# Performance work log

Hardware: AMD Instinct MI355X
Metric: run time of the kernel (lower is better)

Reference implementation:

```python
import jax, jax.numpy as jnp
import numpy as np

IN_DIM = 256
OUT_DIM = 256
B, N, E = 8, 1024, 262144
K_RATIO = 0.5
BN_EPS = 1e-5


def _xavier(key, shape):
    fan_in, fan_out = shape[1], shape[0]
    lim = float(np.sqrt(6.0 / (fan_in + fan_out)))
    return jax.random.uniform(key, shape, jnp.float32, -lim, lim)


def setup_inputs() -> dict:
    key = jax.random.key(0)
    ks = jax.random.split(key, 10)
    x = jax.random.normal(ks[0], (B, N, IN_DIM), jnp.float32)
    edges = jax.random.randint(ks[1], (2, E), 0, B * N, jnp.int64 if jax.config.jax_enable_x64 else jnp.int32)
    return {
        "x": x,
        "edges": edges,
        "att_proj_w": _xavier(ks[2], (OUT_DIM, IN_DIM)),
        "att_proj_b": jnp.zeros((OUT_DIM,), jnp.float32),
        "att_map_w": _xavier(ks[3], (1, OUT_DIM)).reshape(OUT_DIM),
        "pwa_w": _xavier(ks[4], (OUT_DIM, IN_DIM)),
        "pwa_b": jnp.zeros((OUT_DIM,), jnp.float32),
        "pwo_w": _xavier(ks[5], (OUT_DIM, IN_DIM)),
        "pwo_b": jnp.zeros((OUT_DIM,), jnp.float32),
        "bn_gamma": jnp.ones((OUT_DIM,), jnp.float32),
        "bn_beta": jnp.zeros((OUT_DIM,), jnp.float32),
        "y_w": _xavier(ks[6], (1, OUT_DIM)).reshape(OUT_DIM),
        "y_b": jnp.zeros((), jnp.float32),
    }


def reference(x, edges, att_proj_w, att_proj_b, att_map_w, pwa_w, pwa_b,
              pwo_w, pwo_b, bn_gamma, bn_beta, y_w, y_b):
    b, n, d = x.shape
    num_nodes = b * n
    xf = x.reshape(num_nodes, d)
    src, dst = edges[0], edges[1]  # x_j = source, x_i = destination

    # --- GAT message: alpha = att_map(tanh(att_proj(x_i * x_j))) ---
    x_j = xf[src]                                # [E, d]
    x_i = xf[dst]                                # [E, d]
    h = jnp.tanh((x_i * x_j) @ att_proj_w.T + att_proj_b)  # [E, out]
    alpha = h @ att_map_w                        # [E]

    # --- segment softmax over destination nodes ---
    amax = jax.ops.segment_max(alpha, dst, num_segments=num_nodes)
    a = jnp.exp(alpha - amax[dst])
    denom = jax.ops.segment_sum(a, dst, num_segments=num_nodes)
    w = a / (denom[dst] + 1e-16)

    # --- scatter-sum aggregate of alpha * x_j ---
    agg = jax.ops.segment_sum(w[:, None] * x_j, dst, num_segments=num_nodes)  # [num_nodes, d]

    out = agg @ pwa_w.T + pwa_b + xf @ pwo_w.T + pwo_b  # [num_nodes, out]

    # --- BatchNorm1d (training-mode batch stats, biased var) + SELU ---
    mean = out.mean(axis=0)
    var = out.var(axis=0)
    out = (out - mean) * jax.lax.rsqrt(var + BN_EPS) * bn_gamma + bn_beta
    out = jax.nn.selu(out)

    out = out.reshape(b, n, -1)  # [B, N, out]

    # --- GraphPool: top-k by sigmoid score, gate by score ---
    y = jax.nn.sigmoid(out @ y_w + y_b)  # [B, N]
    k = max(int(n * K_RATIO), 1)
    vals, ids = jax.lax.top_k(y, k)      # [B, k]
    x_top = jnp.take_along_axis(out, ids[..., None], axis=1)  # [B, k, out]
    return x_top * vals[..., None]
```

## Files before the change

### kernel.cpp

```cpp
#include <hip/hip_runtime.h>
#include <math.h>

#define NODES 8192
#define NEDGE 262144
#define DIM 256

typedef float f32x16 __attribute__((ext_vector_type(16)));
typedef _Float16 f16x8 __attribute__((ext_vector_type(8)));
typedef unsigned short u16;
typedef u16 u16x8 __attribute__((ext_vector_type(8)));
typedef u16 u16x4 __attribute__((ext_vector_type(4)));
typedef u16 u16x2 __attribute__((ext_vector_type(2)));

__device__ __forceinline__ float fast_tanh(float x) {
    float t = __expf(2.f * x);
    return 1.f - 2.f * __builtin_amdgcn_rcpf(t + 1.f);
}

__device__ __forceinline__ u16 h_bits(_Float16 h) {
    u16 r; __builtin_memcpy(&r, &h, 2); return r;
}

__global__ void k_zero(int* __restrict__ deg) {
    int i = blockIdx.x * blockDim.x + threadIdx.x;
    if (i < NODES) deg[i] = 0;
}

__global__ void k_deg(const int* __restrict__ dst, int* __restrict__ deg) {
    int e = blockIdx.x * blockDim.x + threadIdx.x;
    if (e < NEDGE) atomicAdd(&deg[dst[e]], 1);
}

__global__ void k_scan(const int* __restrict__ deg, int* __restrict__ rowptr,
                       int* __restrict__ cursor) {
    __shared__ int part[256];
    int t = threadIdx.x;
    int base = t * 32;
    int local[32];
    int s = 0;
    for (int i = 0; i < 32; ++i) { local[i] = s; s += deg[base + i]; }
    part[t] = s;
    __syncthreads();
    for (int off = 1; off < 256; off <<= 1) {
        int v = (t >= off) ? part[t - off] : 0;
        __syncthreads();
        part[t] += v;
        __syncthreads();
    }
    int excl = (t == 0) ? 0 : part[t - 1];
    for (int i = 0; i < 32; ++i) {
        int v = excl + local[i];
        rowptr[base + i] = v;
        cursor[base + i] = v;
    }
    if (t == 255) rowptr[NODES] = part[255];
}

__global__ void k_fill(const int* __restrict__ src, const int* __restrict__ dst,
                       int* __restrict__ cursor, int2* __restrict__ sdg) {
    int e = blockIdx.x * blockDim.x + threadIdx.x;
    if (e < NEDGE) {
        int pos = atomicAdd(&cursor[dst[e]], 1);
        sdg[pos] = make_int2(src[e], dst[e]);
    }
}

__global__ void k_wfrag(const float* __restrict__ W, u16* __restrict__ wf) {
    int t = blockIdx.x * blockDim.x + threadIdx.x;
    if (t >= 16 * 4 * 2 * 64) return;
    int lane = t & 63;
    int mt = (t >> 6) & 1;
    int w = (t >> 7) & 3;
    int gks = t >> 9;
    int row = w * 64 + mt * 32 + (lane & 31);
    int k0 = gks * 16 + (lane >> 5) * 8;
    const float* p = W + (size_t)row * DIM + k0;
    u16x8 v1, v2;
#pragma unroll
    for (int j = 0; j < 8; ++j) {
        float f = p[j];
        _Float16 h1 = (_Float16)f;
        _Float16 h2 = (_Float16)((f - (float)h1) * 2048.f);
        v1[j] = h_bits(h1);
        v2[j] = h_bits(h2);
    }
    size_t base = ((size_t)(gks * 4 + w) * 4 + mt * 2) * 512 + lane * 8;
    *(u16x8*)(wf + base)       = v1;
    *(u16x8*)(wf + base + 512) = v2;
}

__global__ void k_wfrag2(const float* __restrict__ Wa, const float* __restrict__ Wo,
                         u16* __restrict__ wf2) {
    int t = blockIdx.x * blockDim.x + threadIdx.x;
    if (t >= 32 * 4 * 2 * 64) return;
    int lane = t & 63;
    int mt = (t >> 6) & 1;
    int w = (t >> 7) & 3;
    int gks = t >> 9;
    const float* W = (gks < 16) ? Wa : Wo;
    int row = w * 64 + mt * 32 + (lane & 31);
    int k0 = (gks & 15) * 16 + (lane >> 5) * 8;
    const float* p = W + (size_t)row * DIM + k0;
    u16x8 v1, v2;
#pragma unroll
    for (int j = 0; j < 8; ++j) {
        float f = p[j];
        _Float16 h1 = (_Float16)f;
        _Float16 h2 = (_Float16)((f - (float)h1) * 2048.f);
        v1[j] = h_bits(h1);
        v2[j] = h_bits(h2);
    }
    size_t base = ((size_t)(gks * 4 + w) * 4 + mt * 2) * 512 + lane * 8;
    *(u16x8*)(wf2 + base)       = v1;
    *(u16x8*)(wf2 + base + 512) = v2;
}

__global__ __launch_bounds__(256, 2) void k_alpha_v10(
    const float* __restrict__ x, const int2* __restrict__ sdg,
    const u16* __restrict__ wf, const float* __restrict__ bias,
    const float* __restrict__ amap, float* __restrict__ alpha_pos)
{
    __shared__ u16 p_lds[2][64][256];
    const int tid = threadIdx.x;
    const int w = tid >> 6;
    const int lane = tid & 63;
    const int l31 = lane & 31;
    const int g2 = lane >> 5;
    const int bid = blockIdx.x;
    const int wg = (bid & 7) * 512 + (bid >> 3);
    const int e0 = wg * 64;
    const int ebase = e0 + w * 16;
    const unsigned swz = ((unsigned)(l31 & 7)) << 4;

    f32x16 accM[2][2], accC[2][2];
#pragma unroll
    for (int mt = 0; mt < 2; ++mt)
#pragma unroll
        for (int nt = 0; nt < 2; ++nt) { accM[mt][nt] = (f32x16)0.f; accC[mt][nt] = (f32x16)0.f; }

    f16x8 afA[2][2], afB[2][2];
    float2 raA[2], rbA[2], raB[2], rbB[2];

#define PREFA(DST, GKS) { \
    const u16* pb_ = wf + ((size_t)((GKS) * 4 + w) * 4) * 512 + lane * 8; \
    _Pragma("unroll") for (int mt_ = 0; mt_ < 2; ++mt_) \
    _Pragma("unroll") for (int pl_ = 0; pl_ < 2; ++pl_) \
        DST[mt_][pl_] = *(const f16x8*)(const void*)(pb_ + (mt_ * 2 + pl_) * 512); }

#define SLOAD(PH, G, RA, RB) { \
    int2 sd0_ = sdg[ebase + (G) * 2]; \
    int2 sd1_ = sdg[ebase + (G) * 2 + 1]; \
    RA[0] = *(const float2*)(x + (size_t)sd0_.x * DIM + (PH) * 128 + lane * 2); \
    RB[0] = *(const float2*)(x + (size_t)sd0_.y * DIM + (PH) * 128 + lane * 2); \
    RA[1] = *(const float2*)(x + (size_t)sd1_.x * DIM + (PH) * 128 + lane * 2); \
    RB[1] = *(const float2*)(x + (size_t)sd1_.y * DIM + (PH) * 128 + lane * 2); }

#define SWRITE(PH, G, RA, RB) { \
    _Pragma("unroll") for (int j_ = 0; j_ < 2; ++j_) { \
        const int le_ = w * 16 + (G) * 2 + j_; \
        float p0_ = RA[j_].x * RB[j_].x; \
        float p1_ = RA[j_].y * RB[j_].y; \
        _Float16 h10_ = (_Float16)p0_; \
        _Float16 h11_ = (_Float16)p1_; \
        _Float16 h20_ = (_Float16)((p0_ - (float)h10_) * 2048.f); \
        _Float16 h21_ = (_Float16)((p1_ - (float)h11_) * 2048.f); \
        u16x2 v1_, v2_; \
        v1_[0] = h_bits(h10_); v1_[1] = h_bits(h11_); \
        v2_[0] = h_bits(h20_); v2_[1] = h_bits(h21_); \
        const unsigned off_ = ((unsigned)((PH) * 256 + lane * 4)) ^ (((unsigned)(le_ & 7)) << 4); \
        *(u16x2*)((char*)&p_lds[0][le_][0] + off_) = v1_; \
        *(u16x2*)((char*)&p_lds[1][le_][0] + off_) = v2_; } }

#define KSTEP(GKS) { \
    if ((GKS) + 1 < 16) { \
        if ((GKS) & 1) { PREFA(afA, (GKS) + 1) } else { PREFA(afB, (GKS) + 1) } \
    } \
    f16x8 bfr[2][2]; \
    _Pragma("unroll") for (int nt_ = 0; nt_ < 2; ++nt_) { \
        const int en_ = nt_ * 32 + l31; \
        const unsigned off_ = ((unsigned)((GKS) * 32 + g2 * 16)) ^ swz; \
        _Pragma("unroll") for (int pl_ = 0; pl_ < 2; ++pl_) \
            bfr[nt_][pl_] = *(const f16x8*)(const void*)((const char*)&p_lds[pl_][en_][0] + off_); \
    } \
    _Pragma("unroll") for (int mt_ = 0; mt_ < 2; ++mt_) \
    _Pragma("unroll") for (int nt_ = 0; nt_ < 2; ++nt_) { \
        f16x8 a1_ = ((GKS) & 1) ? afB[mt_][0] : afA[mt_][0]; \
        f16x8 a2_ = ((GKS) & 1) ? afB[mt_][1] : afA[mt_][1]; \
        accM[mt_][nt_] = __builtin_amdgcn_mfma_f32_32x32x16_f16(a1_, bfr[nt_][0], accM[mt_][nt_], 0, 0, 0); \
        accC[mt_][nt_] = __builtin_amdgcn_mfma_f32_32x32x16_f16(a1_, bfr[nt_][1], accC[mt_][nt_], 0, 0, 0); \
        accC[mt_][nt_] = __builtin_amdgcn_mfma_f32_32x32x16_f16(a2_, bfr[nt_][0], accC[mt_][nt_], 0, 0, 0); } }

    PREFA(afA, 0)
    SLOAD(0, 0, raA, rbA)
    SLOAD(0, 1, raB, rbB)
    SWRITE(0, 0, raA, rbA)
    SLOAD(0, 2, raA, rbA)
    SWRITE(0, 1, raB, rbB)
    SLOAD(0, 3, raB, rbB)
    SWRITE(0, 2, raA, rbA)
    SLOAD(0, 4, raA, rbA)
    SWRITE(0, 3, raB, rbB)
    SLOAD(0, 5, raB, rbB)
    SWRITE(0, 4, raA, rbA)
    SLOAD(0, 6, raA, rbA)
    SWRITE(0, 5, raB, rbB)
    SLOAD(0, 7, raB, rbB)
    SWRITE(0, 6, raA, rbA)
    SWRITE(0, 7, raB, rbB)
    __syncthreads();

    SLOAD(1, 0, raA, rbA)
    KSTEP(0)
    SLOAD(1, 1, raB, rbB)
    SWRITE(1, 0, raA, rbA)
    KSTEP(1)
    SLOAD(1, 2, raA, rbA)
    SWRITE(1, 1, raB, rbB)
    KSTEP(2)
    SLOAD(1, 3, raB, rbB)
    SWRITE(1, 2, raA, rbA)
    KSTEP(3)
    SLOAD(1, 4, raA, rbA)
    SWRITE(1, 3, raB, rbB)
    KSTEP(4)
    SLOAD(1, 5, raB, rbB)
    SWRITE(1, 4, raA, rbA)
    KSTEP(5)
    SLOAD(1, 6, raA, rbA)
    SWRITE(1, 5, raB, rbB)
    KSTEP(6)
    SLOAD(1, 7, raB, rbB)
    SWRITE(1, 6, raA, rbA)
    KSTEP(7)
    SWRITE(1, 7, raB, rbB)
    __syncthreads();
    KSTEP(8)
    KSTEP(9)
    KSTEP(10)
    KSTEP(11)
    KSTEP(12)
    KSTEP(13)
    KSTEP(14)
    KSTEP(15)
#undef SLOAD
#undef SWRITE
#undef KSTEP
#undef PREFA

    float part[2] = {0.f, 0.f};
#pragma unroll
    for (int mt = 0; mt < 2; ++mt)
#pragma unroll
        for (int r = 0; r < 16; ++r) {
            int o = 64 * w + 32 * mt + (r & 3) + 8 * (r >> 2) + 4 * g2;
            float bo = bias[o], ao = amap[o];
#pragma unroll
            for (int nt = 0; nt < 2; ++nt) {
                float h = accM[mt][nt][r] + accC[mt][nt][r] * 4.8828125e-4f;
                part[nt] += ao * fast_tanh(h + bo);
            }
        }
    __syncthreads();
    float* red = (float*)(void*)p_lds;
#pragma unroll
    for (int nt = 0; nt < 2; ++nt) {
        float p = part[nt];
        p += __shfl_xor(p, 32);
        if (lane < 32) red[w * 64 + nt * 32 + lane] = p;
    }
    __syncthreads();
    if (tid < 64) alpha_pos[e0 + tid] = red[tid] + red[64 + tid] + red[128 + tid] + red[192 + tid];
}

__global__ void k_aggregate(
    const float* __restrict__ x, const float* __restrict__ alpha_pos,
    const int* __restrict__ rowptr, const int2* __restrict__ sdg,
    float* __restrict__ agg)
{
    int gw = (blockIdx.x * blockDim.x + threadIdx.x) >> 6;
    int lane = threadIdx.x & 63;
    if (gw >= NODES) return;
    int start = rowptr[gw], end = rowptr[gw + 1];
    int deg = end - start;
    float m = -INFINITY;
    for (int i = lane; i < deg; i += 64) m = fmaxf(m, alpha_pos[start + i]);
#pragma unroll
    for (int off = 32; off > 0; off >>= 1) m = fmaxf(m, __shfl_xor(m, off));
    float ssum = 0.f;
    for (int i = lane; i < deg; i += 64) ssum += expf(alpha_pos[start + i] - m);
#pragma unroll
    for (int off = 32; off > 0; off >>= 1) ssum += __shfl_xor(ssum, off);
    float a0 = 0.f, a1 = 0.f, a2 = 0.f, a3 = 0.f;
    int i = 0;
    for (; i + 4 <= deg; i += 4) {
        float w0 = expf(alpha_pos[start + i]     - m);
        float w1 = expf(alpha_pos[start + i + 1] - m);
        float w2 = expf(alpha_pos[start + i + 2] - m);
        float w3 = expf(alpha_pos[start + i + 3] - m);
        int r0 = sdg[start + i].x;
        int r1 = sdg[start + i + 1].x;
        int r2 = sdg[start + i + 2].x;
        int r3 = sdg[start + i + 3].x;
        float4 v0 = *(const float4*)(x + (size_t)r0 * DIM + lane * 4);
        float4 v1 = *(const float4*)(x + (size_t)r1 * DIM + lane * 4);
        float4 v2 = *(const float4*)(x + (size_t)r2 * DIM + lane * 4);
        float4 v3 = *(const float4*)(x + (size_t)r3 * DIM + lane * 4);
        a0 += w0 * v0.x + w1 * v1.x + w2 * v2.x + w3 * v3.x;
        a1 += w0 * v0.y + w1 * v1.y + w2 * v2.y + w3 * v3.y;
        a2 += w0 * v0.z + w1 * v1.z + w2 * v2.z + w3 * v3.z;
        a3 += w0 * v0.w + w1 * v1.w + w2 * v2.w + w3 * v3.w;
    }
    for (; i < deg; ++i) {
        float wgt = expf(alpha_pos[start + i] - m);
        int r = sdg[start + i].x;
        const float4 v = *(const float4*)(x + (size_t)r * DIM + lane * 4);
        a0 += wgt * v.x; a1 += wgt * v.y; a2 += wgt * v.z; a3 += wgt * v.w;
    }
    float inv = 1.f / (ssum + 1e-16f);
    float4 r; r.x = a0 * inv; r.y = a1 * inv; r.z = a2 * inv; r.w = a3 * inv;
    *(float4*)(agg + (size_t)gw * DIM + lane * 4) = r;
}

__global__ __launch_bounds__(256, 2) void k_out_mfma(
    const float* __restrict__ agg, const float* __restrict__ x,
    const u16* __restrict__ wf2, const float* __restrict__ ba,
    const float* __restrict__ bo, float* __restrict__ outb)
{
    __shared__ u16 p_lds[2][64][256];
    const int tid = threadIdx.x;
    const int w = tid >> 6;
    const int lane = tid & 63;
    const int l31 = lane & 31;
    const int g2 = lane >> 5;
    const int n0 = blockIdx.x * 64;
    const unsigned swz = ((unsigned)(l31 & 7)) << 4;

    f32x16 accM[2][2], accC[2][2];
#pragma unroll
    for (int mt = 0; mt < 2; ++mt)
#pragma unroll
        for (int nt = 0; nt < 2; ++nt) { accM[mt][nt] = (f32x16)0.f; accC[mt][nt] = (f32x16)0.f; }

    f16x8 afA[2][2], afB[2][2];

#define PREFA2(DST, GKS) { \
    const u16* pb_ = wf2 + ((size_t)((GKS) * 4 + w) * 4) * 512 + lane * 8; \
    _Pragma("unroll") for (int mt_ = 0; mt_ < 2; ++mt_) \
    _Pragma("unroll") for (int pl_ = 0; pl_ < 2; ++pl_) \
        DST[mt_][pl_] = *(const f16x8*)(const void*)(pb_ + (mt_ * 2 + pl_) * 512); }

#define OSTAGE(SRC) { \
    _Pragma("unroll") for (int i_ = 0; i_ < 16; ++i_) { \
        const int ln_ = w * 16 + i_; \
        float4 v_ = *(const float4*)((SRC) + (size_t)(n0 + ln_) * DIM + lane * 4); \
        float pv_[4] = {v_.x, v_.y, v_.z, v_.w}; \
        u16x4 v1_, v2_; \
        _Pragma("unroll") for (int j_ = 0; j_ < 4; ++j_) { \
            float f_ = pv_[j_]; \
            _Float16 h1_ = (_Float16)f_; \
            _Float16 h2_ = (_Float16)((f_ - (float)h1_) * 2048.f); \
            v1_[j_] = h_bits(h1_); v2_[j_] = h_bits(h2_); } \
        const unsigned off_ = ((unsigned)(lane * 8)) ^ (((unsigned)(ln_ & 7)) << 4); \
        *(u16x4*)((char*)&p_lds[0][ln_][0] + off_) = v1_; \
        *(u16x4*)((char*)&p_lds[1][ln_][0] + off_) = v2_; } }

#define OKSTEP(GKS) { \
    if ((GKS) + 1 < 32) { \
        if ((GKS) & 1) { PREFA2(afA, (GKS) + 1) } else { PREFA2(afB, (GKS) + 1) } \
    } \
    f16x8 bfr[2][2]; \
    _Pragma("unroll") for (int nt_ = 0; nt_ < 2; ++nt_) { \
        const int en_ = nt_ * 32 + l31; \
        const unsigned off_ = ((unsigned)(((GKS) & 15) * 32 + g2 * 16)) ^ swz; \
        _Pragma("unroll") for (int pl_ = 0; pl_ < 2; ++pl_) \
            bfr[nt_][pl_] = *(const f16x8*)(const void*)((const char*)&p_lds[pl_][en_][0] + off_); \
    } \
    _Pragma("unroll") for (int mt_ = 0; mt_ < 2; ++mt_) \
    _Pragma("unroll") for (int nt_ = 0; nt_ < 2; ++nt_) { \
        f16x8 a1_ = ((GKS) & 1) ? afB[mt_][0] : afA[mt_][0]; \
        f16x8 a2_ = ((GKS) & 1) ? afB[mt_][1] : afA[mt_][1]; \
        accM[mt_][nt_] = __builtin_amdgcn_mfma_f32_32x32x16_f16(a1_, bfr[nt_][0], accM[mt_][nt_], 0, 0, 0); \
        accC[mt_][nt_] = __builtin_amdgcn_mfma_f32_32x32x16_f16(a1_, bfr[nt_][1], accC[mt_][nt_], 0, 0, 0); \
        accC[mt_][nt_] = __builtin_amdgcn_mfma_f32_32x32x16_f16(a2_, bfr[nt_][0], accC[mt_][nt_], 0, 0, 0); } }

    PREFA2(afA, 0)
    OSTAGE(agg)
    __syncthreads();
    OKSTEP(0)  OKSTEP(1)  OKSTEP(2)  OKSTEP(3)
    OKSTEP(4)  OKSTEP(5)  OKSTEP(6)  OKSTEP(7)
    OKSTEP(8)  OKSTEP(9)  OKSTEP(10) OKSTEP(11)
    OKSTEP(12) OKSTEP(13) OKSTEP(14) OKSTEP(15)
    __syncthreads();
    OSTAGE(x)
    __syncthreads();
    OKSTEP(16) OKSTEP(17) OKSTEP(18) OKSTEP(19)
    OKSTEP(20) OKSTEP(21) OKSTEP(22) OKSTEP(23)
    OKSTEP(24) OKSTEP(25) OKSTEP(26) OKSTEP(27)
    OKSTEP(28) OKSTEP(29) OKSTEP(30) OKSTEP(31)
#undef OSTAGE
#undef OKSTEP
#undef PREFA2

    __syncthreads();
    float* Cs = (float*)(void*)p_lds;
#pragma unroll
    for (int mt = 0; mt < 2; ++mt)
#pragma unroll
        for (int r = 0; r < 16; ++r) {
            int o = 64 * w + 32 * mt + (r & 3) + 8 * (r >> 2) + 4 * g2;
            float bs = ba[o] + bo[o];
#pragma unroll
            for (int nt = 0; nt < 2; ++nt) {
                int col = nt * 32 + l31;
                float hv = accM[mt][nt][r] + accC[mt][nt][r] * 4.8828125e-4f + bs;
                unsigned ob = ((unsigned)(col * 1024 + o * 4)) ^ (((unsigned)(col & 31)) << 4);
                *(float*)((char*)Cs + ob) = hv;
            }
        }
    __syncthreads();
#pragma unroll
    for (int i = 0; i < 16; ++i) {
        int ln = w * 16 + i;
        unsigned rb = ((unsigned)(ln * 1024 + lane * 16)) ^ (((unsigned)(ln & 31)) << 4);
        float4 val = *(const float4*)((const char*)Cs + rb);
        *(float4*)(outb + (size_t)(n0 + ln) * DIM + lane * 4) = val;
    }
}

__global__ void k_colstat(const float* __restrict__ outb, double* __restrict__ psum,
                          double* __restrict__ psq) {
    int g = blockIdx.x, t = threadIdx.x;
    double s = 0.0, q = 0.0;
    const float* p = outb + (size_t)g * 256 * DIM + t;
    for (int r = 0; r < 256; ++r) { double v = (double)p[(size_t)r * DIM]; s += v; q += v * v; }
    psum[g * DIM + t] = s;
    psq[g * DIM + t] = q;
}

__global__ void k_bnparam(const double* __restrict__ psum, const double* __restrict__ psq,
                          const float* __restrict__ gamma, const float* __restrict__ beta,
                          float* __restrict__ scale, float* __restrict__ shift) {
    int t = threadIdx.x;
    double s = 0.0, q = 0.0;
    for (int g = 0; g < 32; ++g) { s += psum[g * DIM + t]; q += psq[g * DIM + t]; }
    double mean = s / (double)NODES;
    double var = q / (double)NODES - mean * mean;
    float sc = (float)((double)gamma[t] / sqrt(var + 1e-5));
    scale[t] = sc;
    shift[t] = (float)((double)beta[t] - mean * (double)sc);
}

__global__ void k_bnselu(float* __restrict__ outb, const float* __restrict__ scale,
                         const float* __restrict__ shift, const float* __restrict__ yw,
                         const float* __restrict__ yb, float* __restrict__ y) {
    int gw = (blockIdx.x * blockDim.x + threadIdx.x) >> 6;
    int lane = threadIdx.x & 63;
    if (gw >= NODES) return;
    float4 v  = *(const float4*)(outb + (size_t)gw * DIM + lane * 4);
    float4 sc = *(const float4*)(scale + lane * 4);
    float4 sh = *(const float4*)(shift + lane * 4);
    const float SL = 1.0507009873554805f, SA = 1.6732632423543772f;
    float4 o;
    o.x = v.x * sc.x + sh.x;
    o.y = v.y * sc.y + sh.y;
    o.z = v.z * sc.z + sh.z;
    o.w = v.w * sc.w + sh.w;
    o.x = (o.x > 0.f) ? SL * o.x : SL * SA * expm1f(o.x);
    o.y = (o.y > 0.f) ? SL * o.y : SL * SA * expm1f(o.y);
    o.z = (o.z > 0.f) ? SL * o.z : SL * SA * expm1f(o.z);
    o.w = (o.w > 0.f) ? SL * o.w : SL * SA * expm1f(o.w);
    *(float4*)(outb + (size_t)gw * DIM + lane * 4) = o;
    float4 w = *(const float4*)(yw + lane * 4);
    float z = o.x * w.x + o.y * w.y + o.z * w.z + o.w * w.w;
#pragma unroll
    for (int off = 32; off > 0; off >>= 1) z += __shfl_xor(z, off);
    if (lane == 0) y[gw] = 1.f / (1.f + expf(-(z + yb[0])));
}

__global__ void k_topk(const float* __restrict__ y, float* __restrict__ svals,
                       int* __restrict__ sidx) {
    __shared__ float v[1024];
    __shared__ int  id[1024];
    int b = blockIdx.x, t = threadIdx.x;
    v[t] = y[b * 1024 + t];           id[t] = t;
    v[t + 512] = y[b * 1024 + t + 512]; id[t + 512] = t + 512;
    __syncthreads();
    for (int k = 2; k <= 1024; k <<= 1) {
        for (int j = k >> 1; j > 0; j >>= 1) {
            for (int i = t; i < 1024; i += 512) {
                int l = i ^ j;
                if (l > i) {
                    float vi = v[i], vl = v[l];
                    int ii = id[i], il = id[l];
                    bool precede = (vi > vl) || (vi == vl && ii < il);
                    bool dirDesc = ((i & k) == 0);
                    bool sw = dirDesc ? !precede : precede;
                    if (sw) { v[i] = vl; v[l] = vi; id[i] = il; id[l] = ii; }
                }
            }
            __syncthreads();
        }
    }
    if (t < 512) { svals[b * 512 + t] = v[t]; sidx[b * 512 + t] = id[t]; }
}

__global__ void k_gather(const float* __restrict__ outb, const float* __restrict__ svals,
                         const int* __restrict__ sidx, float* __restrict__ dout) {
    int gw = (blockIdx.x * blockDim.x + threadIdx.x) >> 6;
    int lane = threadIdx.x & 63;
    int b = gw >> 9, r = gw & 511;
    float val = svals[b * 512 + r];
    int idn = sidx[b * 512 + r];
    float4 vv = *(const float4*)(outb + (size_t)(b * 1024 + idn) * DIM + lane * 4);
    vv.x *= val; vv.y *= val; vv.z *= val; vv.w *= val;
    *(float4*)(dout + (size_t)(b * 512 + r) * DIM + lane * 4) = vv;
}

extern "C" void kernel_launch(void* const* d_in, const int* in_sizes, int n_in,
                              void* d_out, int out_size, void* d_ws, size_t ws_size,
                              hipStream_t stream) {
    const float* x     = (const float*)d_in[0];
    const int* edges   = (const int*)d_in[1];
    const float* att_w = (const float*)d_in[2];
    const float* att_b = (const float*)d_in[3];
    const float* amap  = (const float*)d_in[4];
    const float* pwa_w = (const float*)d_in[5];
    const float* pwa_b = (const float*)d_in[6];
    const float* pwo_w = (const float*)d_in[7];
    const float* pwo_b = (const float*)d_in[8];
    const float* gamma = (const float*)d_in[9];
    const float* beta  = (const float*)d_in[10];
    const float* yw    = (const float*)d_in[11];
    const float* yb    = (const float*)d_in[12];
    float* out = (float*)d_out;
    const int* src = edges;
    const int* dst = edges + NEDGE;

    char* ws = (char*)d_ws;
    size_t off = 0;
    auto alloc = [&](size_t b) { void* p = ws + off; off = (off + b + 255) & ~(size_t)255; return p; };
    float* alpha  = (float*)alloc((size_t)NEDGE * 4);
    int2*  sdg    = (int2*)alloc((size_t)NEDGE * 8);
    float* agg    = (float*)alloc((size_t)NODES * DIM * 4);
    float* outb   = (float*)alloc((size_t)NODES * DIM * 4);
    int*   deg    = (int*)alloc(NODES * 4);
    int*   rowptr = (int*)alloc((NODES + 1) * 4);
    int*   cursor = (int*)alloc(NODES * 4);
    double* psum  = (double*)alloc(32 * DIM * 8);
    double* psq   = (double*)alloc(32 * DIM * 8);
    float* scale  = (float*)alloc(DIM * 4);
    float* shift  = (float*)alloc(DIM * 4);
    float* yv     = (float*)alloc(NODES * 4);
    float* svals  = (float*)alloc(8 * 512 * 4);
    int*   sidx   = (int*)alloc(8 * 512 * 4);
    u16*   wf     = (u16*)alloc((size_t)16 * 4 * 4 * 512 * 2);
    u16*   wf2    = (u16*)alloc((size_t)32 * 4 * 4 * 512 * 2);

    k_wfrag<<<32, 256, 0, stream>>>(att_w, wf);
    k_wfrag2<<<64, 256, 0, stream>>>(pwa_w, pwo_w, wf2);
    k_zero<<<NODES / 256, 256, 0, stream>>>(deg);
    k_deg<<<NEDGE / 256, 256, 0, stream>>>(dst, deg);
    k_scan<<<1, 256, 0, stream>>>(deg, rowptr, cursor);
    k_fill<<<NEDGE / 256, 256, 0, stream>>>(src, dst, cursor, sdg);
    k_alpha_v10<<<NEDGE / 64, 256, 0, stream>>>(x, sdg, wf, att_b, amap, alpha);
    k_aggregate<<<NODES / 4, 256, 0, stream>>>(x, alpha, rowptr, sdg, agg);
    k_out_mfma<<<NODES / 64, 256, 0, stream>>>(agg, x, wf2, pwa_b, pwo_b, outb);
    k_colstat<<<32, 256, 0, stream>>>(outb, psum, psq);
    k_bnparam<<<1, 256, 0, stream>>>(psum, psq, gamma, beta, scale, shift);
    k_bnselu<<<NODES / 4, 256, 0, stream>>>(outb, scale, shift, yw, yb, yv);
    k_topk<<<8, 512, 0, stream>>>(yv, svals, sidx);
    k_gather<<<(8 * 512) / 4, 256, 0, stream>>>(outb, svals, sidx, out);
}
```

Before: 276.9 us.

## Halve alpha-kernel LDS staging buffer and stage each K-half in one batch

The alpha kernel's LDS product buffer is cut in half, so only one 128-wide K half is held at a time. Each half is staged by a fully unrolled loop of 16 edge gathers, then consumed by eight MFMA k-steps, with an extra barrier between the halves. This removes the software pipelining that overlapped the second half's gathers with the first half's MFMAs. In exchange it frees LDS for higher occupancy and lets the compiler issue many gathers at once, at the cost of serialising load and compute within a block.

```diff
diff --git a/kernel.cpp b/kernel.cpp
--- a/kernel.cpp
+++ b/kernel.cpp
@@ -115,12 +115,12 @@
     *(u16x8*)(wf2 + base + 512) = v2;
 }
 
-__global__ __launch_bounds__(256, 2) void k_alpha_v10(
+__global__ __launch_bounds__(256, 2) void k_alpha_v11(
     const float* __restrict__ x, const int2* __restrict__ sdg,
     const u16* __restrict__ wf, const float* __restrict__ bias,
     const float* __restrict__ amap, float* __restrict__ alpha_pos)
 {
-    __shared__ u16 p_lds[2][64][256];
+    __shared__ u16 p_lds[2][64][128];
     const int tid = threadIdx.x;
     const int w = tid >> 6;
     const int lane = tid & 63;
@@ -139,7 +139,6 @@
         for (int nt = 0; nt < 2; ++nt) { accM[mt][nt] = (f32x16)0.f; accC[mt][nt] = (f32x16)0.f; }
 
     f16x8 afA[2][2], afB[2][2];
-    float2 raA[2], rbA[2], raB[2], rbB[2];
 
 #define PREFA(DST, GKS) { \
     const u16* pb_ = wf + ((size_t)((GKS) * 4 + w) * 4) * 512 + lane * 8; \
@@ -147,19 +146,13 @@
     _Pragma("unroll") for (int pl_ = 0; pl_ < 2; ++pl_) \
         DST[mt_][pl_] = *(const f16x8*)(const void*)(pb_ + (mt_ * 2 + pl_) * 512); }
 
-#define SLOAD(PH, G, RA, RB) { \
-    int2 sd0_ = sdg[ebase + (G) * 2]; \
-    int2 sd1_ = sdg[ebase + (G) * 2 + 1]; \
-    RA[0] = *(const float2*)(x + (size_t)sd0_.x * DIM + (PH) * 128 + lane * 2); \
-    RB[0] = *(const float2*)(x + (size_t)sd0_.y * DIM + (PH) * 128 + lane * 2); \
-    RA[1] = *(const float2*)(x + (size_t)sd1_.x * DIM + (PH) * 128 + lane * 2); \
-    RB[1] = *(const float2*)(x + (size_t)sd1_.y * DIM + (PH) * 128 + lane * 2); }
-
-#define SWRITE(PH, G, RA, RB) { \
-    _Pragma("unroll") for (int j_ = 0; j_ < 2; ++j_) { \
-        const int le_ = w * 16 + (G) * 2 + j_; \
-        float p0_ = RA[j_].x * RB[j_].x; \
-        float p1_ = RA[j_].y * RB[j_].y; \
+#define STAGE(PH) { \
+    _Pragma("unroll") for (int i_ = 0; i_ < 16; ++i_) { \
+        int2 sd_ = sdg[ebase + i_]; \
+        float2 a_ = *(const float2*)(x + (size_t)sd_.x * DIM + (PH) * 128 + lane * 2); \
+        float2 b_ = *(const float2*)(x + (size_t)sd_.y * DIM + (PH) * 128 + lane * 2); \
+        float p0_ = a_.x * b_.x; \
+        float p1_ = a_.y * b_.y; \
         _Float16 h10_ = (_Float16)p0_; \
         _Float16 h11_ = (_Float16)p1_; \
         _Float16 h20_ = (_Float16)((p0_ - (float)h10_) * 2048.f); \
@@ -167,7 +160,8 @@
         u16x2 v1_, v2_; \
         v1_[0] = h_bits(h10_); v1_[1] = h_bits(h11_); \
         v2_[0] = h_bits(h20_); v2_[1] = h_bits(h21_); \
-        const unsigned off_ = ((unsigned)((PH) * 256 + lane * 4)) ^ (((unsigned)(le_ & 7)) << 4); \
+        const int le_ = w * 16 + i_; \
+        const unsigned off_ = ((unsigned)(lane * 4)) ^ (((unsigned)(le_ & 7)) << 4); \
         *(u16x2*)((char*)&p_lds[0][le_][0] + off_) = v1_; \
         *(u16x2*)((char*)&p_lds[1][le_][0] + off_) = v2_; } }
 
@@ -178,7 +172,7 @@
     f16x8 bfr[2][2]; \
     _Pragma("unroll") for (int nt_ = 0; nt_ < 2; ++nt_) { \
         const int en_ = nt_ * 32 + l31; \
-        const unsigned off_ = ((unsigned)((GKS) * 32 + g2 * 16)) ^ swz; \
+        const unsigned off_ = ((unsigned)(((GKS) & 7) * 32 + g2 * 16)) ^ swz; \
         _Pragma("unroll") for (int pl_ = 0; pl_ < 2; ++pl_) \
             bfr[nt_][pl_] = *(const f16x8*)(const void*)((const char*)&p_lds[pl_][en_][0] + off_); \
     } \
@@ -191,59 +185,16 @@
         accC[mt_][nt_] = __builtin_amdgcn_mfma_f32_32x32x16_f16(a2_, bfr[nt_][0], accC[mt_][nt_], 0, 0, 0); } }
 
     PREFA(afA, 0)
-    SLOAD(0, 0, raA, rbA)
-    SLOAD(0, 1, raB, rbB)
-    SWRITE(0, 0, raA, rbA)
-    SLOAD(0, 2, raA, rbA)
-    SWRITE(0, 1, raB, rbB)
-    SLOAD(0, 3, raB, rbB)
-    SWRITE(0, 2, raA, rbA)
-    SLOAD(0, 4, raA, rbA)
-    SWRITE(0, 3, raB, rbB)
-    SLOAD(0, 5, raB, rbB)
-    SWRITE(0, 4, raA, rbA)
-    SLOAD(0, 6, raA, rbA)
-    SWRITE(0, 5, raB, rbB)
-    SLOAD(0, 7, raB, rbB)
-    SWRITE(0, 6, raA, rbA)
-    SWRITE(0, 7, raB, rbB)
-    __syncthreads();
-
-    SLOAD(1, 0, raA, rbA)
-    KSTEP(0)
-    SLOAD(1, 1, raB, rbB)
-    SWRITE(1, 0, raA, rbA)
-    KSTEP(1)
-    SLOAD(1, 2, raA, rbA)
-    SWRITE(1, 1, raB, rbB)
-    KSTEP(2)
-    SLOAD(1, 3, raB, rbB)
-    SWRITE(1, 2, raA, rbA)
-    KSTEP(3)
-    SLOAD(1, 4, raA, rbA)
-    SWRITE(1, 3, raB, rbB)
-    KSTEP(4)
-    SLOAD(1, 5, raB, rbB)
-    SWRITE(1, 4, raA, rbA)
-    KSTEP(5)
-    SLOAD(1, 6, raA, rbA)
-    SWRITE(1, 5, raB, rbB)
-    KSTEP(6)
-    SLOAD(1, 7, raB, rbB)
-    SWRITE(1, 6, raA, rbA)
-    KSTEP(7)
-    SWRITE(1, 7, raB, rbB)
-    __syncthreads();
-    KSTEP(8)
-    KSTEP(9)
-    KSTEP(10)
-    KSTEP(11)
-    KSTEP(12)
-    KSTEP(13)
-    KSTEP(14)
-    KSTEP(15)
-#undef SLOAD
-#undef SWRITE
+    STAGE(0)
+    __syncthreads();
+    KSTEP(0) KSTEP(1) KSTEP(2) KSTEP(3)
+    KSTEP(4) KSTEP(5) KSTEP(6) KSTEP(7)
+    __syncthreads();
+    STAGE(1)
+    __syncthreads();
+    KSTEP(8)  KSTEP(9)  KSTEP(10) KSTEP(11)
+    KSTEP(12) KSTEP(13) KSTEP(14) KSTEP(15)
+#undef STAGE
 #undef KSTEP
 #undef PREFA
 
@@ -562,7 +513,7 @@
     k_deg<<<NEDGE / 256, 256, 0, stream>>>(dst, deg);
     k_scan<<<1, 256, 0, stream>>>(deg, rowptr, cursor);
     k_fill<<<NEDGE / 256, 256, 0, stream>>>(src, dst, cursor, sdg);
-    k_alpha_v10<<<NEDGE / 64, 256, 0, stream>>>(x, sdg, wf, att_b, amap, alpha);
+    k_alpha_v11<<<NEDGE / 64, 256, 0, stream>>>(x, sdg, wf, att_b, amap, alpha);
     k_aggregate<<<NODES / 4, 256, 0, stream>>>(x, alpha, rowptr, sdg, agg);
     k_out_mfma<<<NODES / 64, 256, 0, stream>>>(agg, x, wf2, pwa_b, pwo_b, outb);
     k_colstat<<<32, 256, 0, stream>>>(outb, psum, psq);
```

New measurement: 274.8 us. Within noise of the previous version (-0.8%).
